# Kernel tuning notes

Hardware: AMD Instinct MI355X
Metric: run time of the kernel (lower is better)

The kernel has to match this reference:

```python
import jax, jax.numpy as jnp
import numpy as np

D_MODEL = 1024
D_HIDDEN = 4096
D_VOCAB = 32000
N_CTX = 2048
N_LAYERS = 8


def setup_inputs() -> dict:
    key = jax.random.key(0)
    ks = jax.random.split(key, 10)
    # scale params by 1/sqrt(fan_in) so softmax/logits are numerically sane
    s = 1.0 / np.sqrt(D_MODEL)
    sh = 1.0 / np.sqrt(D_HIDDEN)
    return {
        "tokens": jax.random.randint(ks[0], (N_CTX,), 0, D_VOCAB),
        "tok_emb": jax.random.normal(ks[1], (D_VOCAB, D_MODEL), jnp.float32) * s,
        "pos_emb": jax.random.normal(ks[2], (N_CTX, D_MODEL), jnp.float32) * s,
        "wqk": jax.random.normal(ks[3], (N_LAYERS, D_MODEL, D_MODEL), jnp.float32) * s,
        "wov": jax.random.normal(ks[4], (N_LAYERS, D_MODEL, D_MODEL), jnp.float32) * s,
        "w_up": jax.random.normal(ks[5], (N_LAYERS, D_HIDDEN, D_MODEL), jnp.float32) * s,
        "b_up": jax.random.normal(ks[6], (N_LAYERS, D_HIDDEN), jnp.float32) * 0.01,
        "w_down": jax.random.normal(ks[7], (N_LAYERS, D_MODEL, D_HIDDEN), jnp.float32) * sh,
        "b_down": jax.random.normal(ks[8], (N_LAYERS, D_MODEL), jnp.float32) * 0.01,
    }


def reference(tokens, tok_emb, pos_emb, wqk, wov, w_up, b_up, w_down, b_down):
    n = tokens.shape[0]
    # token + positional embedding  -> [n, d_model]
    x = tok_emb[tokens] + pos_emb[:n]
    # causal additive mask: -inf strictly above the diagonal
    idx = jnp.arange(n)
    mask = jnp.where(idx[None, :] > idx[:, None], -jnp.inf, 0.0).astype(x.dtype)
    for l in range(wqk.shape[0]):
        # MLP branch: relu(x W_up^T + b_up) W_down^T + b_down
        h = jnp.maximum(x @ w_up[l].T + b_up[l], 0.0) @ w_down[l].T + b_down[l]
        # attention branch: softmax(x Wqk x^T + M) x Wov
        scores = (x @ wqk[l]) @ x.T + mask          # [n, n]
        attn = jax.nn.softmax(scores, axis=-1) @ x @ wov[l]
        x = x + h + attn                             # parallel residual
    # tied unembedding -> logits [n, d_vocab]
    return x @ tok_emb.T
```

## Files before the change

kernel.cpp:

```cpp
#include <hip/hip_runtime.h>
#include <hip/hip_bf16.h>
#include <stdint.h>

#define DM 1024
#define DH 4096
#define DV 32000
#define NC 2048
#define NL 8

typedef float f32x4_t __attribute__((ext_vector_type(4)));
typedef __bf16 bf16x8_t __attribute__((ext_vector_type(8)));
typedef unsigned short u16x4_t __attribute__((ext_vector_type(4)));
typedef unsigned short u16x8_t __attribute__((ext_vector_type(8)));

typedef __attribute__((address_space(1))) void as1_void;
typedef __attribute__((address_space(3))) void as3_void;

__device__ __forceinline__ unsigned short f2bf(float f) {
  unsigned int u = __builtin_bit_cast(unsigned int, f);
  u += 0x7fffu + ((u >> 16) & 1u);
  return (unsigned short)(u >> 16);
}

__device__ __forceinline__ void gload_lds16(const void* g, void* l) {
  __builtin_amdgcn_global_load_lds((as1_void*)(void*)g, (as3_void*)l, 16, 0, 0);
}

__device__ __forceinline__ void cast_tail8(const float* __restrict__ src,
                                           unsigned short* __restrict__ dst,
                                           size_t n, int cidx, int tid) {
  for (size_t i = (size_t)cidx * 2048 + (size_t)tid * 8; i < n;
       i += (size_t)512 * 2048) {
    const float4 a = *reinterpret_cast<const float4*>(src + i);
    const float4 b = *reinterpret_cast<const float4*>(src + i + 4);
    u16x8_t v;
    v[0] = f2bf(a.x); v[1] = f2bf(a.y); v[2] = f2bf(a.z); v[3] = f2bf(a.w);
    v[4] = f2bf(b.x); v[5] = f2bf(b.y); v[6] = f2bf(b.z); v[7] = f2bf(b.w);
    *reinterpret_cast<u16x8_t*>(dst + i) = v;
  }
}

template <int BNT, bool B_FP32, bool SPLIT, bool CAUSAL, bool CAUSAL_K,
          bool HAS_BIAS, bool RELU, bool OUT_BF16>
__device__ __forceinline__ void gemm_body(
    unsigned short* As, unsigned short* Bs, const unsigned short* __restrict__ A,
    const void* __restrict__ Bt, const float* __restrict__ bias,
    void* __restrict__ Cout, int M, int N, int lda, int Ks, int bx, int by,
    int koff, int zslice) {
  constexpr int BK = 64;
  constexpr int BN = BNT;
  constexpr int CPTA = 4;
  constexpr int CPTB = (BN * BK) / 2048;
  constexpr int NF = BN / 32;
  const int t = threadIdx.x;
  const int lane = t & 63;
  const int wid = t >> 6;
  const int wr = wid >> 1, wc = wid & 1;
  const int row0 = by * 128;
  const int col0 = bx * BN;

  if constexpr (CAUSAL) {
    if (col0 > row0 + 127) return;
  }

  int Kend = Ks;
  if constexpr (CAUSAL_K) {
    const int need = row0 + 128 - koff;
    Kend = need <= 0 ? 0 : (need >= Ks ? Ks : ((need + BK - 1) & ~(BK - 1)));
    if constexpr (SPLIT) {
      if (Kend <= 0) return;
    }
  }

  f32x4_t acc[4][NF];
#pragma unroll
  for (int m = 0; m < 4; m++)
#pragma unroll
    for (int n = 0; n < NF; n++) acc[m][n] = (f32x4_t){0.f, 0.f, 0.f, 0.f};

  for (int kt = 0; kt < Kend; kt += BK) {
    __syncthreads();
#pragma unroll
    for (int i = 0; i < CPTA; i++) {
      const int c = i * 256 + t;
      const int r = c >> 3;
      const int ko = ((c & 7) ^ (r & 7)) * 8;
      const unsigned short* g = A + (size_t)(row0 + r) * lda + koff + kt + ko;
      unsigned short* l = &As[(size_t)(i * 256 + wid * 64) * 8];
      gload_lds16(g, l);
    }
    if constexpr (B_FP32) {
      const float* Bf = (const float*)Bt;
#pragma unroll
      for (int i = 0; i < CPTB; i++) {
        const int c = i * 256 + t;
        const int r = c >> 3;
        const int ko = ((c & 7) ^ (r & 7)) * 8;
        const float* g = Bf + (size_t)(col0 + r) * lda + koff + kt + ko;
        const float4 f0 = *reinterpret_cast<const float4*>(g);
        const float4 f1 = *reinterpret_cast<const float4*>(g + 4);
        u16x8_t v;
        v[0] = f2bf(f0.x); v[1] = f2bf(f0.y); v[2] = f2bf(f0.z); v[3] = f2bf(f0.w);
        v[4] = f2bf(f1.x); v[5] = f2bf(f1.y); v[6] = f2bf(f1.z); v[7] = f2bf(f1.w);
        *reinterpret_cast<u16x8_t*>(&Bs[(size_t)c * 8]) = v;
      }
    } else {
      const unsigned short* Bu = (const unsigned short*)Bt;
#pragma unroll
      for (int i = 0; i < CPTB; i++) {
        const int c = i * 256 + t;
        const int r = c >> 3;
        const int ko = ((c & 7) ^ (r & 7)) * 8;
        const unsigned short* g = Bu + (size_t)(col0 + r) * lda + koff + kt + ko;
        unsigned short* l = &Bs[(size_t)(i * 256 + wid * 64) * 8];
        gload_lds16(g, l);
      }
    }
    __syncthreads();

#pragma unroll
    for (int kk = 0; kk < 2; kk++) {
      bf16x8_t av[4], bv[NF];
#pragma unroll
      for (int m = 0; m < 4; m++) {
        const int arow = wr * 64 + m * 16 + (lane & 15);
        const int akc = (kk * 4 + (lane >> 4)) ^ (arow & 7);
        av[m] = __builtin_bit_cast(
            bf16x8_t, *reinterpret_cast<const u16x8_t*>(&As[arow * BK + akc * 8]));
      }
#pragma unroll
      for (int n = 0; n < NF; n++) {
        const int brow = wc * (BN / 2) + n * 16 + (lane & 15);
        const int bkc = (kk * 4 + (lane >> 4)) ^ (brow & 7);
        bv[n] = __builtin_bit_cast(
            bf16x8_t, *reinterpret_cast<const u16x8_t*>(&Bs[brow * BK + bkc * 8]));
      }
#pragma unroll
      for (int m = 0; m < 4; m++)
#pragma unroll
        for (int n = 0; n < NF; n++)
          acc[m][n] = __builtin_amdgcn_mfma_f32_16x16x32_bf16(av[m], bv[n],
                                                              acc[m][n], 0, 0, 0);
    }
  }

#pragma unroll
  for (int m = 0; m < 4; m++) {
    const int rbase = row0 + wr * 64 + m * 16 + (lane >> 4) * 4;
#pragma unroll
    for (int n = 0; n < NF; n++) {
      const int col = col0 + wc * (BN / 2) + n * 16 + (lane & 15);
      if constexpr (SPLIT) {
        float* out = (float*)Cout + (size_t)zslice * M * N;
#pragma unroll
        for (int j = 0; j < 4; j++)
          out[(size_t)(rbase + j) * N + col] = acc[m][n][j];
      } else {
        float bval = 0.0f;
        if constexpr (HAS_BIAS) bval = bias[col];
#pragma unroll
        for (int j = 0; j < 4; j++) {
          float v = acc[m][n][j];
          if constexpr (HAS_BIAS) v += bval;
          if constexpr (RELU) v = fmaxf(v, 0.0f);
          const size_t idx = (size_t)(rbase + j) * N + col;
          if constexpr (OUT_BF16)
            ((unsigned short*)Cout)[idx] = f2bf(v);
          else
            __builtin_nontemporal_store(v, (float*)Cout + idx);
        }
      }
    }
  }
}

__device__ __forceinline__ void super_decode(int idx, int gy, int& bx, int& by) {
  const int s = idx >> 4;
  const int u = idx & 15;
  const int sgy = gy >> 2;
  const int sx = s / sgy;
  const int sy = s - sx * sgy;
  bx = sx * 4 + (u & 3);
  by = sy * 4 + (u >> 2);
}

template <int BNT, bool B_FP32, bool SPLIT, bool CAUSAL, bool CAUSAL_K,
          bool HAS_BIAS, bool RELU, bool OUT_BF16>
__global__ __launch_bounds__(256) void gemm_nt(
    const unsigned short* __restrict__ A, const void* __restrict__ Bt,
    const float* __restrict__ bias, void* __restrict__ Cout, int M, int N,
    int lda, int Ks) {
  __shared__ __attribute__((aligned(16))) unsigned short As[128 * 64];
  __shared__ __attribute__((aligned(16))) unsigned short Bs[BNT * 64];
  const int gx = gridDim.x, gy = gridDim.y;
  const int nwg = gx * gy;
  const int orig = blockIdx.y * gx + blockIdx.x;
  const int qq = nwg >> 3, rr = nwg & 7;
  const int xc = orig & 7, ii = orig >> 3;
  const int wgid = (xc < rr ? xc * (qq + 1) : rr * (qq + 1) + (xc - rr) * qq) + ii;
  int bx, by;
  super_decode(wgid, gy, bx, by);
  gemm_body<BNT, B_FP32, SPLIT, CAUSAL, CAUSAL_K, HAS_BIAS, RELU, OUT_BF16>(
      As, Bs, A, Bt, bias, Cout, M, N, lda, Ks, bx, by,
      SPLIT ? blockIdx.z * Ks : 0, blockIdx.z);
}

__global__ __launch_bounds__(256) void gemm_ov_res(
    const unsigned short* __restrict__ A, const unsigned short* __restrict__ Bt,
    float* __restrict__ x, unsigned short* __restrict__ xb,
    unsigned short* __restrict__ xT, const float* __restrict__ dp,
    const float* __restrict__ bd) {
  __shared__ __attribute__((aligned(16))) unsigned short As[128 * 64];
  __shared__ __attribute__((aligned(16))) unsigned short Bs[64 * 64];
  const int gx = gridDim.x, gy = gridDim.y;
  const int nwg = gx * gy;
  const int orig = blockIdx.y * gx + blockIdx.x;
  const int qq = nwg >> 3, rr = nwg & 7;
  const int xc = orig & 7, ii = orig >> 3;
  const int wgid = (xc < rr ? xc * (qq + 1) : rr * (qq + 1) + (xc - rr) * qq) + ii;
  int bx, by;
  super_decode(wgid, gy, bx, by);

  const int t = threadIdx.x;
  const int lane = t & 63;
  const int wid = t >> 6;
  const int wr = wid >> 1, wc = wid & 1;
  const int row0 = by * 128;
  const int col0 = bx * 64;

  f32x4_t acc[4][2];
#pragma unroll
  for (int m = 0; m < 4; m++)
#pragma unroll
    for (int n = 0; n < 2; n++) acc[m][n] = (f32x4_t){0.f, 0.f, 0.f, 0.f};

  for (int kt = 0; kt < DM; kt += 64) {
    __syncthreads();
#pragma unroll
    for (int i = 0; i < 4; i++) {
      const int c = i * 256 + t;
      const int r = c >> 3;
      const int ko = ((c & 7) ^ (r & 7)) * 8;
      const unsigned short* g = A + (size_t)(row0 + r) * DM + kt + ko;
      unsigned short* l = &As[(size_t)(i * 256 + wid * 64) * 8];
      gload_lds16(g, l);
    }
#pragma unroll
    for (int i = 0; i < 2; i++) {
      const int c = i * 256 + t;
      const int r = c >> 3;
      const int ko = ((c & 7) ^ (r & 7)) * 8;
      const unsigned short* g = Bt + (size_t)(col0 + r) * DM + kt + ko;
      unsigned short* l = &Bs[(size_t)(i * 256 + wid * 64) * 8];
      gload_lds16(g, l);
    }
    __syncthreads();

#pragma unroll
    for (int kk = 0; kk < 2; kk++) {
      bf16x8_t av[4], bv[2];
#pragma unroll
      for (int m = 0; m < 4; m++) {
        const int arow = wr * 64 + m * 16 + (lane & 15);
        const int akc = (kk * 4 + (lane >> 4)) ^ (arow & 7);
        av[m] = __builtin_bit_cast(
            bf16x8_t, *reinterpret_cast<const u16x8_t*>(&As[arow * 64 + akc * 8]));
      }
#pragma unroll
      for (int n = 0; n < 2; n++) {
        const int brow = wc * 32 + n * 16 + (lane & 15);
        const int bkc = (kk * 4 + (lane >> 4)) ^ (brow & 7);
        bv[n] = __builtin_bit_cast(
            bf16x8_t, *reinterpret_cast<const u16x8_t*>(&Bs[brow * 64 + bkc * 8]));
      }
#pragma unroll
      for (int m = 0; m < 4; m++)
#pragma unroll
        for (int n = 0; n < 2; n++)
          acc[m][n] = __builtin_amdgcn_mfma_f32_16x16x32_bf16(av[m], bv[n],
                                                              acc[m][n], 0, 0, 0);
    }
  }

  const size_t nMD = (size_t)NC * DM;
#pragma unroll
  for (int m = 0; m < 4; m++) {
    const int rbase = row0 + wr * 64 + m * 16 + (lane >> 4) * 4;
#pragma unroll
    for (int n = 0; n < 2; n++) {
      const int col = col0 + wc * 32 + n * 16 + (lane & 15);
      const float bval = bd[col];
      u16x4_t ot;
#pragma unroll
      for (int j = 0; j < 4; j++) {
        const size_t idx = (size_t)(rbase + j) * DM + col;
        float v = acc[m][n][j] + x[idx] + bval;
#pragma unroll
        for (int s = 0; s < 4; s++) v += dp[(size_t)s * nMD + idx];
        x[idx] = v;
        const unsigned short o = f2bf(v);
        xb[idx] = o;
        ot[j] = o;
      }
      *reinterpret_cast<u16x4_t*>(&xT[(size_t)col * NC + rbase]) = ot;
    }
  }
}

__global__ __launch_bounds__(256) void fused_up_q(
    const unsigned short* __restrict__ xb, const unsigned short* __restrict__ wupB,
    const float* __restrict__ bup, unsigned short* __restrict__ h1,
    const unsigned short* __restrict__ wqkT, unsigned short* __restrict__ qb,
    const float* __restrict__ c0s, unsigned short* __restrict__ c0d, size_t c0n,
    const float* __restrict__ c1s, unsigned short* __restrict__ c1d, size_t c1n) {
  __shared__ __attribute__((aligned(16))) unsigned short As[128 * 64];
  __shared__ __attribute__((aligned(16))) unsigned short Bs[64 * 64];
  const int orig = blockIdx.x;
  const int xc = orig & 7, ii = orig >> 3;
  int bx, by;
  if (ii < 128) {
    const int idx = xc * 128 + ii;
    super_decode(idx, 16, bx, by);
    gemm_body<64, false, false, false, false, true, true, true>(
        As, Bs, xb, wupB, bup, h1, NC, DH, DM, DM, bx, by, 0, 0);
  } else if (ii < 160) {
    const int idx = xc * 32 + (ii - 128);
    super_decode(idx, 16, bx, by);
    gemm_body<64, false, false, false, false, false, false, true>(
        As, Bs, xb, wqkT, nullptr, qb, NC, DM, DM, DM, bx, by, 0, 0);
  } else {
    const int cidx = xc * 64 + (ii - 160);
    cast_tail8(c0s, c0d, c0n, cidx, threadIdx.x);
    cast_tail8(c1s, c1d, c1n, cidx, threadIdx.x);
  }
}

__global__ __launch_bounds__(256) void fused_down_sc(
    const unsigned short* __restrict__ h1, const unsigned short* __restrict__ wdownB,
    float* __restrict__ dpart, const unsigned short* __restrict__ qb,
    const unsigned short* __restrict__ xbv, float* __restrict__ spool,
    const float* __restrict__ c0s, unsigned short* __restrict__ c0d, size_t c0n,
    const float* __restrict__ c1s, unsigned short* __restrict__ c1d, size_t c1n) {
  __shared__ __attribute__((aligned(16))) unsigned short As[128 * 64];
  __shared__ __attribute__((aligned(16))) unsigned short Bs[64 * 64];
  const int orig = blockIdx.x;
  const int xc = orig & 7, ii = orig >> 3;
  if (ii < 128) {
    const int idx = xc * 128 + ii;
    const int z = idx >> 8;
    int bx, by;
    super_decode(idx & 255, 16, bx, by);
    gemm_body<64, false, true, false, false, false, false, false>(
        As, Bs, h1, wdownB, nullptr, dpart, NC, DM, DH, DH / 4, bx, by,
        z * (DH / 4), z);
  } else if (ii < 256) {
    const int idx = xc * 128 + (ii - 128);
    const int z = idx >> 9;
    int bx, by;
    super_decode(idx & 511, 16, bx, by);
    gemm_body<64, false, true, true, false, false, false, false>(
        As, Bs, qb, xbv, nullptr, spool, NC, NC, DM, DM / 2, bx, by,
        z * (DM / 2), z);
  } else {
    const int cidx = xc * 64 + (ii - 256);
    cast_tail8(c0s, c0d, c0n, cidx, threadIdx.x);
    cast_tail8(c1s, c1d, c1n, cidx, threadIdx.x);
  }
}

__global__ __launch_bounds__(256) void cast3_f32_bf16(
    const float* __restrict__ in0, unsigned short* __restrict__ out0, size_t n0,
    const float* __restrict__ in1, unsigned short* __restrict__ out1, size_t n1,
    const float* __restrict__ in2, unsigned short* __restrict__ out2, size_t n2,
    int gper) {
  const int seg = blockIdx.x / gper;
  const int lb = blockIdx.x - seg * gper;
  const float* in = seg == 0 ? in0 : (seg == 1 ? in1 : in2);
  unsigned short* out = seg == 0 ? out0 : (seg == 1 ? out1 : out2);
  const size_t n = seg == 0 ? n0 : (seg == 1 ? n1 : n2);
  const size_t stride = (size_t)gper * 256 * 8;
  for (size_t i = ((size_t)lb * 256 + threadIdx.x) * 8; i < n; i += stride) {
    const float4 a = *reinterpret_cast<const float4*>(in + i);
    const float4 b = *reinterpret_cast<const float4*>(in + i + 4);
    u16x8_t v;
    v[0] = f2bf(a.x); v[1] = f2bf(a.y); v[2] = f2bf(a.z); v[3] = f2bf(a.w);
    v[4] = f2bf(b.x); v[5] = f2bf(b.y); v[6] = f2bf(b.z); v[7] = f2bf(b.w);
    *reinterpret_cast<u16x8_t*>(out + i) = v;
  }
}

__global__ __launch_bounds__(256) void embed_kernel(
    const int* __restrict__ tokens, const float* __restrict__ tok_emb,
    const float* __restrict__ pos_emb, float* __restrict__ x,
    unsigned short* __restrict__ xb) {
  const int i = blockIdx.x;
  const int tok = tokens[i];
  const float* te = tok_emb + (size_t)tok * DM;
  const float* pe = pos_emb + (size_t)i * DM;
  float* xr = x + (size_t)i * DM;
  unsigned short* xbr = xb + (size_t)i * DM;
  const int j = threadIdx.x * 4;
  const float4 a = *reinterpret_cast<const float4*>(te + j);
  const float4 b = *reinterpret_cast<const float4*>(pe + j);
  float4 v;
  v.x = a.x + b.x; v.y = a.y + b.y; v.z = a.z + b.z; v.w = a.w + b.w;
  *reinterpret_cast<float4*>(xr + j) = v;
  u16x4_t o;
  o[0] = f2bf(v.x); o[1] = f2bf(v.y); o[2] = f2bf(v.z); o[3] = f2bf(v.w);
  *reinterpret_cast<u16x4_t*>(xbr + j) = o;
}

__global__ void transpose_cast_dual(const float* __restrict__ in0,
                                    unsigned short* __restrict__ out0,
                                    const float* __restrict__ in1,
                                    unsigned short* __restrict__ out1, int R,
                                    int C, int ZSPLIT) {
  __shared__ float tile[32][33];
  const int z = blockIdx.z;
  const float* in = (z < ZSPLIT) ? in0 : in1;
  unsigned short* out = (z < ZSPLIT) ? out0 : out1;
  const int zl = (z < ZSPLIT) ? z : z - ZSPLIT;
  const size_t lo = (size_t)zl * R * C;
  const int x = blockIdx.x * 32 + threadIdx.x;
#pragma unroll
  for (int i = threadIdx.y; i < 32; i += 8) {
    const int y = blockIdx.y * 32 + i;
    tile[i][threadIdx.x] = in[lo + (size_t)y * C + x];
  }
  __syncthreads();
  const int ox = blockIdx.y * 32 + threadIdx.x;
#pragma unroll
  for (int i = threadIdx.y; i < 32; i += 8) {
    const int oy = blockIdx.x * 32 + i;
    out[lo + (size_t)oy * R + ox] = f2bf(tile[threadIdx.x][i]);
  }
}

__global__ void transpose_u16(const unsigned short* __restrict__ in,
                              unsigned short* __restrict__ out, int R, int C) {
  __shared__ unsigned short tile[32][33];
  const int x = blockIdx.x * 32 + threadIdx.x;
#pragma unroll
  for (int i = threadIdx.y; i < 32; i += 8) {
    const int y = blockIdx.y * 32 + i;
    tile[i][threadIdx.x] = in[(size_t)y * C + x];
  }
  __syncthreads();
  const int ox = blockIdx.y * 32 + threadIdx.x;
#pragma unroll
  for (int i = threadIdx.y; i < 32; i += 8) {
    const int oy = blockIdx.x * 32 + i;
    out[(size_t)oy * R + ox] = tile[threadIdx.x][i];
  }
}

__global__ __launch_bounds__(256) void softmax_split2(
    const float* __restrict__ p0, const float* __restrict__ p1,
    unsigned short* __restrict__ P, int n) {
  __shared__ float srow[NC];
  __shared__ float sred[4];
  const int i = blockIdx.x;
  const int valid = i + 1;
  const int wlimit = (i & ~127) + 128;
  const int t = threadIdx.x;
  const int wid = t >> 6, lane = t & 63;
  const size_t ro = (size_t)i * n;
  for (int j = t; j < valid; j += 256) srow[j] = p0[ro + j] + p1[ro + j];
  __syncthreads();

  float m = -3.0e38f;
  for (int j = t; j < valid; j += 256) m = fmaxf(m, srow[j]);
#pragma unroll
  for (int o = 32; o > 0; o >>= 1) m = fmaxf(m, __shfl_xor(m, o, 64));
  if (lane == 0) sred[wid] = m;
  __syncthreads();
  m = fmaxf(fmaxf(sred[0], sred[1]), fmaxf(sred[2], sred[3]));
  __syncthreads();

  float s = 0.f;
  for (int j = t; j < valid; j += 256) s += __expf(srow[j] - m);
#pragma unroll
  for (int o = 32; o > 0; o >>= 1) s += __shfl_xor(s, o, 64);
  if (lane == 0) sred[wid] = s;
  __syncthreads();
  s = sred[0] + sred[1] + sred[2] + sred[3];
  const float inv = 1.0f / s;

  unsigned short* prow = P + ro;
  for (int j = t; j < wlimit; j += 256)
    prow[j] = (j < valid) ? f2bf(__expf(srow[j] - m) * inv) : (unsigned short)0;
}

__global__ __launch_bounds__(256) void softmax_causal(
    const float* __restrict__ S, unsigned short* __restrict__ P, int n) {
  __shared__ float srow[NC];
  __shared__ float sred[4];
  const int i = blockIdx.x;
  const int valid = i + 1;
  const int t = threadIdx.x;
  const int wid = t >> 6, lane = t & 63;
  const size_t ro = (size_t)i * n;
  for (int j = t; j < valid; j += 256) srow[j] = S[ro + j];
  __syncthreads();
  float m = -3.0e38f;
  for (int j = t; j < valid; j += 256) m = fmaxf(m, srow[j]);
#pragma unroll
  for (int o = 32; o > 0; o >>= 1) m = fmaxf(m, __shfl_xor(m, o, 64));
  if (lane == 0) sred[wid] = m;
  __syncthreads();
  m = fmaxf(fmaxf(sred[0], sred[1]), fmaxf(sred[2], sred[3]));
  __syncthreads();
  float s = 0.f;
  for (int j = t; j < valid; j += 256) s += __expf(srow[j] - m);
#pragma unroll
  for (int o = 32; o > 0; o >>= 1) s += __shfl_xor(s, o, 64);
  if (lane == 0) sred[wid] = s;
  __syncthreads();
  s = sred[0] + sred[1] + sred[2] + sred[3];
  const float inv = 1.0f / s;
  unsigned short* prow = P + ro;
  for (int j = t; j < n; j += 256)
    prow[j] = (j < valid) ? f2bf(__expf(srow[j] - m) * inv) : (unsigned short)0;
}

__global__ __launch_bounds__(256) void reduce_pv_causal(
    const float* __restrict__ part, unsigned short* __restrict__ out, size_t n,
    size_t stride) {
  const size_t i = ((size_t)blockIdx.x * 256 + threadIdx.x) * 4;
  if (i >= n) return;
  const int row = (int)(i >> 10);
  const int nsl = (row >> 9) + 1;
  float4 v = *reinterpret_cast<const float4*>(part + i);
  for (int s = 1; s < nsl; s++) {
    const float4 w = *reinterpret_cast<const float4*>(part + (size_t)s * stride + i);
    v.x += w.x; v.y += w.y; v.z += w.z; v.w += w.w;
  }
  u16x4_t o;
  o[0] = f2bf(v.x); o[1] = f2bf(v.y); o[2] = f2bf(v.z); o[3] = f2bf(v.w);
  *reinterpret_cast<u16x4_t*>(out + i) = o;
}

__global__ __launch_bounds__(256) void residual_tiled(
    float* __restrict__ x, unsigned short* __restrict__ xb,
    unsigned short* __restrict__ xT, const float* __restrict__ dp,
    const float* __restrict__ op, const float* __restrict__ bd) {
  __shared__ unsigned short tile[32][33];
  const int tx = threadIdx.x;
  const int ty = threadIdx.y;
  const int col0 = blockIdx.x * 32;
  const int row0 = blockIdx.y * 32;
  const size_t n = (size_t)NC * DM;
  const int row = row0 + ty;
  const int col = col0 + tx * 4;
  const size_t idx = (size_t)row * DM + col;

  float4 v = *reinterpret_cast<const float4*>(x + idx);
  const float4 b = *reinterpret_cast<const float4*>(bd + col);
  v.x += b.x; v.y += b.y; v.z += b.z; v.w += b.w;
#pragma unroll
  for (int s = 0; s < 4; s++) {
    const float4 w = *reinterpret_cast<const float4*>(dp + (size_t)s * n + idx);
    v.x += w.x; v.y += w.y; v.z += w.z; v.w += w.w;
  }
#pragma unroll
  for (int s = 0; s < 2; s++) {
    const float4 w = *reinterpret_cast<const float4*>(op + (size_t)s * n + idx);
    v.x += w.x; v.y += w.y; v.z += w.z; v.w += w.w;
  }
  *reinterpret_cast<float4*>(x + idx) = v;
  u16x4_t o;
  o[0] = f2bf(v.x); o[1] = f2bf(v.y); o[2] = f2bf(v.z); o[3] = f2bf(v.w);
  *reinterpret_cast<u16x4_t*>(xb + idx) = o;
  tile[ty][tx * 4 + 0] = o[0];
  tile[ty][tx * 4 + 1] = o[1];
  tile[ty][tx * 4 + 2] = o[2];
  tile[ty][tx * 4 + 3] = o[3];
  __syncthreads();

  const int t = ty * 8 + tx;
  const int wc = t >> 5;
  const int wr = t & 31;
#pragma unroll
  for (int j = 0; j < 4; j++) {
    const int c = wc + j * 8;
    xT[(size_t)(col0 + c) * NC + row0 + wr] = tile[wr][c];
  }
}

__global__ __launch_bounds__(256) void residual_kernel(
    float* __restrict__ x, const float* __restrict__ hd,
    const float* __restrict__ attn, unsigned short* __restrict__ xb, int n) {
  const int idx = blockIdx.x * 256 + threadIdx.x;
  if (idx < n) {
    const float v = x[idx] + hd[idx] + attn[idx];
    x[idx] = v;
    xb[idx] = f2bf(v);
  }
}

extern "C" void kernel_launch(void* const* d_in, const int* in_sizes, int n_in,
                              void* d_out, int out_size, void* d_ws,
                              size_t ws_size, hipStream_t stream) {
  const int* tokens = (const int*)d_in[0];
  const float* tok_emb = (const float*)d_in[1];
  const float* pos_emb = (const float*)d_in[2];
  const float* wqk = (const float*)d_in[3];
  const float* wov = (const float*)d_in[4];
  const float* w_up = (const float*)d_in[5];
  const float* b_up = (const float*)d_in[6];
  const float* w_down = (const float*)d_in[7];
  const float* b_down = (const float*)d_in[8];
  float* logits = (float*)d_out;

  uint8_t* base = (uint8_t*)d_ws;
  size_t used = 0;
  auto alloc = [&](size_t bytes) -> void* {
    const size_t ab = (bytes + 255) & ~(size_t)255;
    if (used + ab > ws_size) return (void*)0;
    void* r = base + used;
    used += ab;
    return r;
  };

  float* x = (float*)alloc((size_t)NC * DM * 4);
  unsigned short* xb = (unsigned short*)alloc((size_t)NC * DM * 2);
  unsigned short* h1 = (unsigned short*)alloc((size_t)NC * DH * 2);
  unsigned short* qb = (unsigned short*)alloc((size_t)NC * DM * 2);
  unsigned short* Pb = (unsigned short*)alloc((size_t)NC * NC * 2);
  unsigned short* xT = (unsigned short*)alloc((size_t)NC * DM * 2);
  unsigned short* ab = (unsigned short*)alloc((size_t)NC * DM * 2);
  unsigned short* wqkT = (unsigned short*)alloc((size_t)NL * DM * DM * 2);
  unsigned short* wovT = (unsigned short*)alloc((size_t)NL * DM * DM * 2);
  float* hd = (float*)alloc((size_t)NC * DM * 4);
  float* attn = (float*)alloc((size_t)NC * DM * 4);
  float* scores = (float*)alloc((size_t)NC * NC * 4);
  float* dpart = (float*)alloc((size_t)4 * NC * DM * 4);
  float* opart = (float*)alloc((size_t)2 * NC * DM * 4);
  float* pool = (float*)alloc((size_t)2 * NC * NC * 4);
  unsigned short* wupB = (unsigned short*)alloc((size_t)NL * DH * DM * 2);
  unsigned short* wdownB = (unsigned short*)alloc((size_t)NL * DM * DH * 2);
  unsigned short* tokB = (unsigned short*)alloc((size_t)DV * DM * 2);

  const bool split_en = (dpart && opart && pool);
  const bool have_wbf = (wupB && wdownB);
  const bool have_tok = (tokB != 0);
  const bool fused_en = split_en && have_wbf;

  const dim3 tb(32, 8);
  transpose_cast_dual<<<dim3(DM / 32, DM / 32, 2 * NL), tb, 0, stream>>>(
      wqk, wqkT, wov, wovT, DM, DM, NL);
  if (fused_en) {
    cast3_f32_bf16<<<2 * 1024, 256, 0, stream>>>(
        w_up, wupB, (size_t)DH * DM, w_down, wdownB, (size_t)DM * DH,
        nullptr, nullptr, 0, 1024);
  } else if (have_wbf && have_tok) {
    cast3_f32_bf16<<<3 * 2048, 256, 0, stream>>>(
        w_up, wupB, (size_t)NL * DH * DM, w_down, wdownB, (size_t)NL * DM * DH,
        tok_emb, tokB, (size_t)DV * DM, 2048);
  }
  embed_kernel<<<NC, 256, 0, stream>>>(tokens, tok_emb, pos_emb, x, xb);
  transpose_u16<<<dim3(DM / 32, NC / 32), tb, 0, stream>>>(xb, xT, NC, DM);

  const size_t nMD = (size_t)NC * DM;
  const size_t tokQ = (size_t)DV * DM / (2 * NL);

  for (int l = 0; l < NL; l++) {
    if (fused_en) {
      const bool nw = (l + 1 < NL);
      const float* u0s = nw ? w_up + (size_t)(l + 1) * DH * DM : nullptr;
      unsigned short* u0d = nw ? wupB + (size_t)(l + 1) * DH * DM : nullptr;
      const size_t u0n = nw ? (size_t)DH * DM : 0;
      const float* d0s = nw ? w_down + (size_t)(l + 1) * DM * DH : nullptr;
      unsigned short* d0d = nw ? wdownB + (size_t)(l + 1) * DM * DH : nullptr;
      const size_t d0n = nw ? (size_t)DM * DH : 0;
      const float* t0s = have_tok ? tok_emb + (size_t)l * 2 * tokQ : nullptr;
      unsigned short* t0d = have_tok ? tokB + (size_t)l * 2 * tokQ : nullptr;
      const float* t1s = have_tok ? tok_emb + (size_t)l * 2 * tokQ + tokQ : nullptr;
      unsigned short* t1d = have_tok ? tokB + (size_t)l * 2 * tokQ + tokQ : nullptr;
      const size_t tn = have_tok ? tokQ : 0;

      fused_up_q<<<1792, 256, 0, stream>>>(
          xb, wupB + (size_t)l * DH * DM, b_up + (size_t)l * DH, h1,
          wqkT + (size_t)l * DM * DM, qb, u0s, u0d, u0n, t0s, t0d, tn);
      fused_down_sc<<<2560, 256, 0, stream>>>(
          h1, wdownB + (size_t)l * DM * DH, dpart, qb, xb, pool, d0s, d0d,
          d0n, t1s, t1d, tn);
      softmax_split2<<<NC, 256, 0, stream>>>(pool, pool + (size_t)NC * NC, Pb, NC);
      gemm_nt<64, false, true, false, true, false, false, false>
          <<<dim3(DM / 64, NC / 128, 4), 256, 0, stream>>>(
              Pb, xT, nullptr, pool, NC, DM, NC, NC / 4);
      reduce_pv_causal<<<(nMD / 4 + 255) / 256, 256, 0, stream>>>(pool, ab, nMD, nMD);
      gemm_ov_res<<<dim3(DM / 64, NC / 128), 256, 0, stream>>>(
          ab, wovT + (size_t)l * DM * DM, x, xb, xT, dpart,
          b_down + (size_t)l * DM);
    } else {
      gemm_nt<64, true, false, false, false, true, true, true>
          <<<dim3(DH / 64, NC / 128), 256, 0, stream>>>(
              xb, w_up + (size_t)l * DH * DM, b_up + (size_t)l * DH, h1, NC, DH, DM, DM);
      gemm_nt<64, true, false, false, false, true, false, false>
          <<<dim3(DM / 64, NC / 128), 256, 0, stream>>>(
              h1, w_down + (size_t)l * DM * DH, b_down + (size_t)l * DM, hd, NC, DM, DH, DH);
      gemm_nt<64, false, false, false, false, false, false, true>
          <<<dim3(DM / 64, NC / 128), 256, 0, stream>>>(
              xb, wqkT + (size_t)l * DM * DM, nullptr, qb, NC, DM, DM, DM);

      if (split_en) {
        gemm_nt<64, false, true, true, false, false, false, false>
            <<<dim3(NC / 64, NC / 128, 2), 256, 0, stream>>>(
                qb, xb, nullptr, pool, NC, NC, DM, DM / 2);
        softmax_split2<<<NC, 256, 0, stream>>>(pool, pool + (size_t)NC * NC, Pb, NC);
        gemm_nt<64, false, true, false, true, false, false, false>
            <<<dim3(DM / 64, NC / 128, 4), 256, 0, stream>>>(
                Pb, xT, nullptr, pool, NC, DM, NC, NC / 4);
        reduce_pv_causal<<<(nMD / 4 + 255) / 256, 256, 0, stream>>>(pool, ab, nMD, nMD);
        gemm_nt<64, false, true, false, false, false, false, false>
            <<<dim3(DM / 64, NC / 128, 2), 256, 0, stream>>>(
                ab, wovT + (size_t)l * DM * DM, nullptr, opart, NC, DM, DM, DM / 2);
        residual_tiled<<<dim3(DM / 32, NC / 32), dim3(8, 32), 0, stream>>>(
            x, xb, xT, dpart, opart, b_down + (size_t)l * DM);
      } else {
        gemm_nt<64, false, false, true, false, false, false, false>
            <<<dim3(NC / 64, NC / 128), 256, 0, stream>>>(
                qb, xb, nullptr, scores, NC, NC, DM, DM);
        softmax_causal<<<NC, 256, 0, stream>>>(scores, Pb, NC);
        transpose_u16<<<dim3(DM / 32, NC / 32), tb, 0, stream>>>(xb, xT, NC, DM);
        gemm_nt<64, false, false, false, true, false, false, true>
            <<<dim3(DM / 64, NC / 128), 256, 0, stream>>>(
                Pb, xT, nullptr, ab, NC, DM, NC, NC);
        gemm_nt<64, false, false, false, false, false, false, false>
            <<<dim3(DM / 64, NC / 128), 256, 0, stream>>>(
                ab, wovT + (size_t)l * DM * DM, nullptr, attn, NC, DM, DM, DM);
        residual_kernel<<<(int)(nMD / 256), 256, 0, stream>>>(x, hd, attn, xb, (int)nMD);
      }
    }
  }

  if (have_tok && (fused_en || have_wbf))
    gemm_nt<64, false, false, false, false, false, false, false>
        <<<dim3(DV / 64, NC / 128), 256, 0, stream>>>(
            xb, tokB, nullptr, logits, NC, DV, DM, DM);
  else
    gemm_nt<64, true, false, false, false, false, false, false>
        <<<dim3(DV / 64, NC / 128), 256, 0, stream>>>(
            xb, tok_emb, nullptr, logits, NC, DV, DM, DM);
}
```

Before: 1.288 ms.

## Fold weight pre-casts into per-layer fused kernels and read fp32 on layer zero

```diff
diff --git a/kernel.cpp b/kernel.cpp
--- a/kernel.cpp
+++ b/kernel.cpp
@@ -307,12 +307,15 @@
   }
 }
 
+template <bool WUP32>
 __global__ __launch_bounds__(256) void fused_up_q(
-    const unsigned short* __restrict__ xb, const unsigned short* __restrict__ wupB,
+    const unsigned short* __restrict__ xb, const void* __restrict__ wup,
     const float* __restrict__ bup, unsigned short* __restrict__ h1,
     const unsigned short* __restrict__ wqkT, unsigned short* __restrict__ qb,
     const float* __restrict__ c0s, unsigned short* __restrict__ c0d, size_t c0n,
-    const float* __restrict__ c1s, unsigned short* __restrict__ c1d, size_t c1n) {
+    const float* __restrict__ c1s, unsigned short* __restrict__ c1d, size_t c1n,
+    const float* __restrict__ tr0s, unsigned short* __restrict__ tr0d,
+    const float* __restrict__ tr1s, unsigned short* __restrict__ tr1d) {
   __shared__ __attribute__((aligned(16))) unsigned short As[128 * 64];
   __shared__ __attribute__((aligned(16))) unsigned short Bs[64 * 64];
   const int orig = blockIdx.x;
@@ -321,22 +324,49 @@
   if (ii < 128) {
     const int idx = xc * 128 + ii;
     super_decode(idx, 16, bx, by);
-    gemm_body<64, false, false, false, false, true, true, true>(
-        As, Bs, xb, wupB, bup, h1, NC, DH, DM, DM, bx, by, 0, 0);
+    gemm_body<64, WUP32, false, false, false, true, true, true>(
+        As, Bs, xb, wup, bup, h1, NC, DH, DM, DM, bx, by, 0, 0);
   } else if (ii < 160) {
     const int idx = xc * 32 + (ii - 128);
     super_decode(idx, 16, bx, by);
     gemm_body<64, false, false, false, false, false, false, true>(
         As, Bs, xb, wqkT, nullptr, qb, NC, DM, DM, DM, bx, by, 0, 0);
-  } else {
+  } else if (ii < 224) {
     const int cidx = xc * 64 + (ii - 160);
     cast_tail8(c0s, c0d, c0n, cidx, threadIdx.x);
     cast_tail8(c1s, c1d, c1n, cidx, threadIdx.x);
-  }
-}
-
+  } else {
+    if (tr0s == nullptr) return;
+    float* tf = (float*)As;
+    const int tb = xc * 32 + (ii - 224);
+    const int tx = threadIdx.x & 31;
+    const int ty = threadIdx.x >> 5;
+#pragma unroll 1
+    for (int jj = 0; jj < 8; jj++) {
+      const int j = tb * 8 + jj;
+      const float* src = (j < 1024) ? tr0s : tr1s;
+      unsigned short* dst = (j < 1024) ? tr0d : tr1d;
+      const int tile = j & 1023;
+      const int tX = tile & 31, tY = tile >> 5;
+      __syncthreads();
+#pragma unroll
+      for (int i = 0; i < 4; i++) {
+        const int r = ty + i * 8;
+        tf[r * 33 + tx] = src[(size_t)(tY * 32 + r) * DM + tX * 32 + tx];
+      }
+      __syncthreads();
+#pragma unroll
+      for (int i = 0; i < 4; i++) {
+        const int r = ty + i * 8;
+        dst[(size_t)(tX * 32 + r) * DM + tY * 32 + tx] = f2bf(tf[tx * 33 + r]);
+      }
+    }
+  }
+}
+
+template <bool WDN32>
 __global__ __launch_bounds__(256) void fused_down_sc(
-    const unsigned short* __restrict__ h1, const unsigned short* __restrict__ wdownB,
+    const unsigned short* __restrict__ h1, const void* __restrict__ wdown,
     float* __restrict__ dpart, const unsigned short* __restrict__ qb,
     const unsigned short* __restrict__ xbv, float* __restrict__ spool,
     const float* __restrict__ c0s, unsigned short* __restrict__ c0d, size_t c0n,
@@ -350,8 +380,8 @@
     const int z = idx >> 8;
     int bx, by;
     super_decode(idx & 255, 16, bx, by);
-    gemm_body<64, false, true, false, false, false, false, false>(
-        As, Bs, h1, wdownB, nullptr, dpart, NC, DM, DH, DH / 4, bx, by,
+    gemm_body<64, WDN32, true, false, false, false, false, false>(
+        As, Bs, h1, wdown, nullptr, dpart, NC, DM, DH, DH / 4, bx, by,
         z * (DH / 4), z);
   } else if (ii < 256) {
     const int idx = xc * 128 + (ii - 128);
@@ -647,16 +677,16 @@
   const bool fused_en = split_en && have_wbf;
 
   const dim3 tb(32, 8);
-  transpose_cast_dual<<<dim3(DM / 32, DM / 32, 2 * NL), tb, 0, stream>>>(
-      wqk, wqkT, wov, wovT, DM, DM, NL);
   if (fused_en) {
-    cast3_f32_bf16<<<2 * 1024, 256, 0, stream>>>(
-        w_up, wupB, (size_t)DH * DM, w_down, wdownB, (size_t)DM * DH,
-        nullptr, nullptr, 0, 1024);
-  } else if (have_wbf && have_tok) {
-    cast3_f32_bf16<<<3 * 2048, 256, 0, stream>>>(
-        w_up, wupB, (size_t)NL * DH * DM, w_down, wdownB, (size_t)NL * DM * DH,
-        tok_emb, tokB, (size_t)DV * DM, 2048);
+    transpose_cast_dual<<<dim3(DM / 32, DM / 32, 2), tb, 0, stream>>>(
+        wqk, wqkT, wov, wovT, DM, DM, 1);
+  } else {
+    transpose_cast_dual<<<dim3(DM / 32, DM / 32, 2 * NL), tb, 0, stream>>>(
+        wqk, wqkT, wov, wovT, DM, DM, NL);
+    if (have_wbf && have_tok)
+      cast3_f32_bf16<<<3 * 2048, 256, 0, stream>>>(
+          w_up, wupB, (size_t)NL * DH * DM, w_down, wdownB, (size_t)NL * DM * DH,
+          tok_emb, tokB, (size_t)DV * DM, 2048);
   }
   embed_kernel<<<NC, 256, 0, stream>>>(tokens, tok_emb, pos_emb, x, xb);
   transpose_u16<<<dim3(DM / 32, NC / 32), tb, 0, stream>>>(xb, xT, NC, DM);
@@ -678,13 +708,27 @@
       const float* t1s = have_tok ? tok_emb + (size_t)l * 2 * tokQ + tokQ : nullptr;
       unsigned short* t1d = have_tok ? tokB + (size_t)l * 2 * tokQ + tokQ : nullptr;
       const size_t tn = have_tok ? tokQ : 0;
-
-      fused_up_q<<<1792, 256, 0, stream>>>(
-          xb, wupB + (size_t)l * DH * DM, b_up + (size_t)l * DH, h1,
-          wqkT + (size_t)l * DM * DM, qb, u0s, u0d, u0n, t0s, t0d, tn);
-      fused_down_sc<<<2560, 256, 0, stream>>>(
-          h1, wdownB + (size_t)l * DM * DH, dpart, qb, xb, pool, d0s, d0d,
-          d0n, t1s, t1d, tn);
+      const float* tr0s = nw ? wqk + (size_t)(l + 1) * DM * DM : nullptr;
+      unsigned short* tr0d = nw ? wqkT + (size_t)(l + 1) * DM * DM : nullptr;
+      const float* tr1s = nw ? wov + (size_t)(l + 1) * DM * DM : nullptr;
+      unsigned short* tr1d = nw ? wovT + (size_t)(l + 1) * DM * DM : nullptr;
+
+      if (l == 0)
+        fused_up_q<true><<<2048, 256, 0, stream>>>(
+            xb, w_up, b_up, h1, wqkT, qb, u0s, u0d, u0n, t0s, t0d, tn,
+            tr0s, tr0d, tr1s, tr1d);
+      else
+        fused_up_q<false><<<2048, 256, 0, stream>>>(
+            xb, wupB + (size_t)l * DH * DM, b_up + (size_t)l * DH, h1,
+            wqkT + (size_t)l * DM * DM, qb, u0s, u0d, u0n, t0s, t0d, tn,
+            tr0s, tr0d, tr1s, tr1d);
+      if (l == 0)
+        fused_down_sc<true><<<2560, 256, 0, stream>>>(
+            h1, w_down, dpart, qb, xb, pool, d0s, d0d, d0n, t1s, t1d, tn);
+      else
+        fused_down_sc<false><<<2560, 256, 0, stream>>>(
+            h1, wdownB + (size_t)l * DM * DH, dpart, qb, xb, pool, d0s, d0d,
+            d0n, t1s, t1d, tn);
       softmax_split2<<<NC, 256, 0, stream>>>(pool, pool + (size_t)NC * NC, Pb, NC);
       gemm_nt<64, false, true, false, true, false, false, false>
           <<<dim3(DM / 64, NC / 128, 4), 256, 0, stream>>>(
@@ -735,7 +779,11 @@
     }
   }
 
-  if (have_tok && (fused_en || have_wbf))
+  if (have_tok && fused_en)
+    gemm_nt<64, false, false, false, false, false, false, false>
+        <<<dim3(DV / 64, NC / 128), 256, 0, stream>>>(
+            xb, tokB, nullptr, logits, NC, DV, DM, DM);
+  else if (have_tok && have_wbf)
     gemm_nt<64, false, false, false, false, false, false, false>
         <<<dim3(DV / 64, NC / 128), 256, 0, stream>>>(
             xb, tokB, nullptr, logits, NC, DV, DM, DM);
```

After: 1.255 ms (median of 2 runs). 1.03x faster.
